# Kernel optimization log

Hardware: AMD Instinct MI355X
Metric: run time of the kernel (lower is better)

Reference implementation:

```python
import jax, jax.numpy as jnp
import numpy as np

MARGIN = 1.0

def setup_inputs() -> dict:
    key = jax.random.key(0)
    k1, k2, k3 = jax.random.split(key, 3)
    B, C, D = 65536, 1000, 512
    x = jax.random.normal(k1, (B, D), dtype=jnp.float32)
    x = x / jnp.linalg.norm(x, axis=1, keepdims=True)  # docstring: ||x||2 = 1
    labels = jax.random.randint(k2, (B,), 0, C, dtype=jnp.int64)
    centers = jax.random.normal(k3, (C, D), dtype=jnp.float32)
    return {"x": x, "labels": labels, "centers": centers}

def reference(x, labels, centers):
    # l2Norm applied to the centers (module is only used when l2Norm is truthy)
    c = centers / jnp.linalg.norm(centers, axis=1, keepdims=True)  # (C, D)
    # cosine distance to every center: one batched GEMM instead of per-sample loop
    dist = 1.0 - jnp.einsum("bd,cd->bc", x, c)                      # (B, C)
    pos = jnp.take_along_axis(dist, labels[:, None], axis=1)[:, 0]  # (B,)
    # min over all classes != label: mask own class with +inf
    same = jnp.arange(c.shape[0])[None, :] == labels[:, None]       # (B, C)
    neg = jnp.min(jnp.where(same, jnp.inf, dist), axis=1)           # (B,)
    # sum of per-sample hinge losses divided by batch size == mean
    return jnp.mean(jax.nn.relu(pos + MARGIN - neg))
```

## Files before the change

kernel.cpp:

```cpp
#include <hip/hip_runtime.h>
#include <stdint.h>

typedef short v8s __attribute__((ext_vector_type(8)));
typedef short v4s __attribute__((ext_vector_type(4)));
typedef float v4f __attribute__((ext_vector_type(4)));

#define BM 128
#define BN 128
#define BK 64
#define POS_INF __builtin_inff()

typedef __attribute__((address_space(3))) unsigned int lds_uint;
typedef const __attribute__((address_space(1))) unsigned int glb_uint;

__device__ __forceinline__ void load16_lds(const void* g, void* l) {
    __builtin_amdgcn_global_load_lds((glb_uint*)g, (lds_uint*)l, 16, 0, 0);
}

__device__ __forceinline__ short f2bf(float f) {
    uint32_t u = __builtin_bit_cast(uint32_t, f);
    u += 0x7fffu + ((u >> 16) & 1u);
    return (short)(u >> 16);
}

__global__ void prep_centers(const float* __restrict__ centers,
                             unsigned short* __restrict__ cbf,
                             int C, int D, float* __restrict__ out) {
    const int row  = blockIdx.x;
    const int lane = threadIdx.x;
    if (row == 0 && lane == 0) out[0] = 0.0f;
    if (row >= C) {
        v4s z = {0, 0, 0, 0};
        for (int d = lane * 4; d < D; d += 256)
            *(v4s*)&cbf[(size_t)row * D + d] = z;
        return;
    }
    const float* src = centers + (size_t)row * D;
    float ss = 0.0f;
    for (int d = lane * 4; d < D; d += 256) {
        v4f f = *(const v4f*)&src[d];
        ss += f.x * f.x + f.y * f.y + f.z * f.z + f.w * f.w;
    }
    #pragma unroll
    for (int off = 32; off; off >>= 1) ss += __shfl_xor(ss, off, 64);
    const float rn = rsqrtf(ss);
    for (int d = lane * 4; d < D; d += 256) {
        v4f f = *(const v4f*)&src[d];
        v4s s;
        s.x = f2bf(f.x * rn); s.y = f2bf(f.y * rn);
        s.z = f2bf(f.z * rn); s.w = f2bf(f.w * rn);
        *(v4s*)&cbf[(size_t)row * D + d] = s;
    }
}

__global__ void convert_x(const float* __restrict__ x,
                          unsigned short* __restrict__ xbf, size_t n) {
    size_t i = ((size_t)blockIdx.x * blockDim.x + threadIdx.x) * 8;
    if (i >= n) return;
    v4f f0 = *(const v4f*)&x[i];
    v4f f1 = *(const v4f*)&x[i + 4];
    v8s s;
    s[0] = f2bf(f0.x); s[1] = f2bf(f0.y); s[2] = f2bf(f0.z); s[3] = f2bf(f0.w);
    s[4] = f2bf(f1.x); s[5] = f2bf(f1.y); s[6] = f2bf(f1.z); s[7] = f2bf(f1.w);
    *(v8s*)&xbf[i] = s;
}

__global__ void gemm_fused(const float* __restrict__ xf,
                           const unsigned short* __restrict__ xbf, int useBf,
                           const unsigned short* __restrict__ cbf,
                           const int* __restrict__ labels,
                           float* __restrict__ pos, float* __restrict__ partial,
                           int Bt, int C, int D, int NT) {
    __shared__ short As[BM * BK];
    __shared__ short Bs[BN * BK];
    __shared__ int   Ls[BM];
    __shared__ float sMinW[2][BM];

    const int t    = threadIdx.x;
    const int nt   = blockIdx.x;
    const int row0 = blockIdx.y * BM;
    const int n0   = nt * BN;

    if (t < BM) Ls[t] = labels[row0 + t];

    const int lane = t & 63;
    const int wave = t >> 6;
    const int wm = wave >> 1, wn = wave & 1;
    const int l15 = lane & 15, q = lane >> 4;

    const int rsub = lane >> 3;
    const int csrc = (lane & 7) ^ rsub;

    v4f acc[4][4];
    #pragma unroll
    for (int i = 0; i < 4; ++i)
        #pragma unroll
        for (int j = 0; j < 4; ++j)
            acc[i][j] = (v4f){0.f, 0.f, 0.f, 0.f};

    const int KT = D / BK;
    for (int kk = 0; kk < KT; ++kk) {
        const int k0 = kk * BK;
        #pragma unroll
        for (int p = 0; p < 4; ++p) {
            const int rbase = wave * 32 + p * 8;
            const unsigned short* g =
                &cbf[(size_t)(n0 + rbase + rsub) * D + k0 + csrc * 8];
            load16_lds(g, &Bs[rbase * BK]);
        }
        if (useBf) {
            #pragma unroll
            for (int p = 0; p < 4; ++p) {
                const int rbase = wave * 32 + p * 8;
                const unsigned short* g =
                    &xbf[(size_t)(row0 + rbase + rsub) * D + k0 + csrc * 8];
                load16_lds(g, &As[rbase * BK]);
            }
        } else {
            #pragma unroll
            for (int p = 0; p < 4; ++p) {
                const int r = (t >> 3) + p * 32;
                const int cs = t & 7;
                const float* src = &xf[(size_t)(row0 + r) * D + k0 + cs * 8];
                v4f f0 = *(const v4f*)&src[0];
                v4f f1 = *(const v4f*)&src[4];
                v8s s;
                s[0] = f2bf(f0.x); s[1] = f2bf(f0.y);
                s[2] = f2bf(f0.z); s[3] = f2bf(f0.w);
                s[4] = f2bf(f1.x); s[5] = f2bf(f1.y);
                s[6] = f2bf(f1.z); s[7] = f2bf(f1.w);
                *(v8s*)&As[r * BK + (cs ^ (r & 7)) * 8] = s;
            }
        }
        __syncthreads();
        #pragma unroll
        for (int ki = 0; ki < BK; ki += 32) {
            const int cbase = ki >> 3;
            v8s a[4], b[4];
            #pragma unroll
            for (int i = 0; i < 4; ++i) {
                const int m = wm * 64 + i * 16 + l15;
                a[i] = *(const v8s*)&As[m * BK + (((cbase + q) ^ (l15 & 7)) * 8)];
            }
            #pragma unroll
            for (int j = 0; j < 4; ++j) {
                const int n = wn * 64 + j * 16 + l15;
                b[j] = *(const v8s*)&Bs[n * BK + (((cbase + q) ^ (l15 & 7)) * 8)];
            }
            #pragma unroll
            for (int i = 0; i < 4; ++i)
                #pragma unroll
                for (int j = 0; j < 4; ++j)
                    acc[i][j] = __builtin_amdgcn_mfma_f32_16x16x32_bf16(
                        a[i], b[j], acc[i][j], 0, 0, 0);
        }
        __syncthreads();
    }

    #pragma unroll
    for (int i = 0; i < 4; ++i) {
        #pragma unroll
        for (int rg = 0; rg < 4; ++rg) {
            const int row_l = wm * 64 + i * 16 + q * 4 + rg;
            const int lab = Ls[row_l];
            float m = POS_INF;
            #pragma unroll
            for (int j = 0; j < 4; ++j) {
                const int col = n0 + wn * 64 + j * 16 + l15;
                const float d = 1.0f - acc[i][j][rg];
                if (col == lab) pos[row0 + row_l] = d;
                else if (col < C) m = fminf(m, d);
            }
            m = fminf(m, __shfl_xor(m, 1, 64));
            m = fminf(m, __shfl_xor(m, 2, 64));
            m = fminf(m, __shfl_xor(m, 4, 64));
            m = fminf(m, __shfl_xor(m, 8, 64));
            if (l15 == 0) sMinW[wn][row_l] = m;
        }
    }
    __syncthreads();
    if (t < BM) {
        const float m = fminf(sMinW[0][t], sMinW[1][t]);
        partial[(size_t)nt * Bt + row0 + t] = m;
    }
}

__global__ void reduce_loss(const float* __restrict__ pos,
                            const float* __restrict__ partial,
                            int Bt, int NT, float margin,
                            float* __restrict__ out) {
    const int r = blockIdx.x * 256 + threadIdx.x;
    float h = 0.0f;
    if (r < Bt) {
        float neg = POS_INF;
        for (int tt = 0; tt < NT; ++tt)
            neg = fminf(neg, partial[(size_t)tt * Bt + r]);
        h = fmaxf(0.0f, pos[r] + margin - neg);
    }
    #pragma unroll
    for (int off = 32; off; off >>= 1) h += __shfl_down(h, off, 64);
    __shared__ float wsum[4];
    const int lane = threadIdx.x & 63, wave = threadIdx.x >> 6;
    if (lane == 0) wsum[wave] = h;
    __syncthreads();
    if (threadIdx.x == 0)
        atomicAdd(out, (wsum[0] + wsum[1] + wsum[2] + wsum[3]) * (1.0f / (float)Bt));
}

extern "C" void kernel_launch(void* const* d_in, const int* in_sizes, int n_in,
                              void* d_out, int out_size, void* d_ws, size_t ws_size,
                              hipStream_t stream) {
    const float* x       = (const float*)d_in[0];
    const int*   labels  = (const int*)d_in[1];
    const float* centers = (const float*)d_in[2];
    float* out = (float*)d_out;

    const int Bt = in_sizes[1];
    const int D  = in_sizes[0] / Bt;
    const int C  = in_sizes[2] / D;
    const int NT = (C + BN - 1) / BN;
    const int CP = NT * BN;

    char* ws = (char*)d_ws;
    unsigned short* cbf = (unsigned short*)ws;
    size_t off = (size_t)CP * D * 2;
    off = (off + 255) & ~(size_t)255;
    float* pos = (float*)(ws + off);      off += (size_t)Bt * 4;
    float* partial = (float*)(ws + off);  off += (size_t)NT * Bt * 4;
    unsigned short* xbf = (unsigned short*)(ws + off);
    const size_t needBig = off + (size_t)Bt * D * 2;
    const int useBf = (ws_size >= needBig) ? 1 : 0;

    prep_centers<<<CP, 64, 0, stream>>>(centers, cbf, C, D, out);
    if (useBf) {
        const size_t n = (size_t)Bt * D;
        convert_x<<<(unsigned)((n / 8 + 255) / 256), 256, 0, stream>>>(x, xbf, n);
    }
    dim3 grid(NT, Bt / BM);
    gemm_fused<<<grid, 256, 0, stream>>>(x, xbf, useBf, cbf, labels, pos, partial,
                                         Bt, C, D, NT);
    reduce_loss<<<(Bt + 255) / 256, 256, 0, stream>>>(pos, partial, Bt, NT, 1.0f, out);
}
```

Before: 298.5 us.

## Remap GEMM blocks per XCD, merge prep kernels, and alias epilogue LDS

The 2D GEMM grid becomes a 1D grid whose block index is decoded so that all eight column tiles of one row block run on the same XCD. Each x tile should then be reused from that XCD's L2 instead of being fetched by eight different XCDs. The centers-normalisation and x-to-bf16 conversion kernels are merged into one launch, with center rows now handled one per wave. The label and min-reduction scratch arrays reuse the GEMM's LDS tiles after the main loop, which shrinks static LDS. The new mapping hardcodes eight column tiles and needs the row-block count to be a multiple of eight, so it holds only for shapes like C=1000.

After: 290.3 us. 2.8% less time.

```diff
diff --git a/kernel.cpp b/kernel.cpp
--- a/kernel.cpp
+++ b/kernel.cpp
@@ -23,46 +23,51 @@
     return (short)(u >> 16);
 }
 
-__global__ void prep_centers(const float* __restrict__ centers,
-                             unsigned short* __restrict__ cbf,
-                             int C, int D, float* __restrict__ out) {
-    const int row  = blockIdx.x;
-    const int lane = threadIdx.x;
-    if (row == 0 && lane == 0) out[0] = 0.0f;
-    if (row >= C) {
-        v4s z = {0, 0, 0, 0};
-        for (int d = lane * 4; d < D; d += 256)
-            *(v4s*)&cbf[(size_t)row * D + d] = z;
-        return;
-    }
-    const float* src = centers + (size_t)row * D;
-    float ss = 0.0f;
-    for (int d = lane * 4; d < D; d += 256) {
-        v4f f = *(const v4f*)&src[d];
-        ss += f.x * f.x + f.y * f.y + f.z * f.z + f.w * f.w;
-    }
-    #pragma unroll
-    for (int off = 32; off; off >>= 1) ss += __shfl_xor(ss, off, 64);
-    const float rn = rsqrtf(ss);
-    for (int d = lane * 4; d < D; d += 256) {
-        v4f f = *(const v4f*)&src[d];
-        v4s s;
-        s.x = f2bf(f.x * rn); s.y = f2bf(f.y * rn);
-        s.z = f2bf(f.z * rn); s.w = f2bf(f.w * rn);
-        *(v4s*)&cbf[(size_t)row * D + d] = s;
-    }
-}
-
-__global__ void convert_x(const float* __restrict__ x,
-                          unsigned short* __restrict__ xbf, size_t n) {
-    size_t i = ((size_t)blockIdx.x * blockDim.x + threadIdx.x) * 8;
-    if (i >= n) return;
-    v4f f0 = *(const v4f*)&x[i];
-    v4f f1 = *(const v4f*)&x[i + 4];
-    v8s s;
-    s[0] = f2bf(f0.x); s[1] = f2bf(f0.y); s[2] = f2bf(f0.z); s[3] = f2bf(f0.w);
-    s[4] = f2bf(f1.x); s[5] = f2bf(f1.y); s[6] = f2bf(f1.z); s[7] = f2bf(f1.w);
-    *(v8s*)&xbf[i] = s;
+__global__ void prep(const float* __restrict__ centers,
+                     unsigned short* __restrict__ cbf,
+                     int C, int D, int CP, int CB,
+                     const float* __restrict__ x,
+                     unsigned short* __restrict__ xbf, size_t nx,
+                     float* __restrict__ out) {
+    const int b = blockIdx.x;
+    const int t = threadIdx.x;
+    if (b == 0 && t == 0) out[0] = 0.0f;
+    if (b < CB) {
+        const int wave = t >> 6, lane = t & 63;
+        const int row = b * 4 + wave;
+        if (row >= CP) return;
+        if (row >= C) {
+            v4s z = {0, 0, 0, 0};
+            for (int d = lane * 4; d < D; d += 256)
+                *(v4s*)&cbf[(size_t)row * D + d] = z;
+            return;
+        }
+        const float* src = centers + (size_t)row * D;
+        float ss = 0.0f;
+        for (int d = lane * 4; d < D; d += 256) {
+            v4f f = *(const v4f*)&src[d];
+            ss += f.x * f.x + f.y * f.y + f.z * f.z + f.w * f.w;
+        }
+        #pragma unroll
+        for (int off = 32; off; off >>= 1) ss += __shfl_xor(ss, off, 64);
+        const float rn = rsqrtf(ss);
+        for (int d = lane * 4; d < D; d += 256) {
+            v4f f = *(const v4f*)&src[d];
+            v4s s;
+            s.x = f2bf(f.x * rn); s.y = f2bf(f.y * rn);
+            s.z = f2bf(f.z * rn); s.w = f2bf(f.w * rn);
+            *(v4s*)&cbf[(size_t)row * D + d] = s;
+        }
+    } else {
+        const size_t i = ((size_t)(b - CB) * 256 + t) * 8;
+        if (i >= nx) return;
+        v4f f0 = *(const v4f*)&x[i];
+        v4f f1 = *(const v4f*)&x[i + 4];
+        v8s s;
+        s[0] = f2bf(f0.x); s[1] = f2bf(f0.y); s[2] = f2bf(f0.z); s[3] = f2bf(f0.w);
+        s[4] = f2bf(f1.x); s[5] = f2bf(f1.y); s[6] = f2bf(f1.z); s[7] = f2bf(f1.w);
+        *(v8s*)&xbf[i] = s;
+    }
 }
 
 __global__ void gemm_fused(const float* __restrict__ xf,
@@ -73,15 +78,15 @@
                            int Bt, int C, int D, int NT) {
     __shared__ short As[BM * BK];
     __shared__ short Bs[BN * BK];
-    __shared__ int   Ls[BM];
-    __shared__ float sMinW[2][BM];
-
-    const int t    = threadIdx.x;
-    const int nt   = blockIdx.x;
-    const int row0 = blockIdx.y * BM;
+
+    const int t   = threadIdx.x;
+    const int bid = blockIdx.x;
+    const int xcd = bid & 7;
+    const int per = bid >> 3;
+    const int rowblk = (per >> 3) * 8 + xcd;
+    const int nt     = per & 7;
+    const int row0 = rowblk * BM;
     const int n0   = nt * BN;
-
-    if (t < BM) Ls[t] = labels[row0 + t];
 
     const int lane = t & 63;
     const int wave = t >> 6;
@@ -157,6 +162,11 @@
         __syncthreads();
     }
 
+    int*   Ls    = (int*)As;
+    float* sMinW = (float*)Bs;
+    if (t < BM) Ls[t] = labels[row0 + t];
+    __syncthreads();
+
     #pragma unroll
     for (int i = 0; i < 4; ++i) {
         #pragma unroll
@@ -175,12 +185,12 @@
             m = fminf(m, __shfl_xor(m, 2, 64));
             m = fminf(m, __shfl_xor(m, 4, 64));
             m = fminf(m, __shfl_xor(m, 8, 64));
-            if (l15 == 0) sMinW[wn][row_l] = m;
+            if (l15 == 0) sMinW[wn * BM + row_l] = m;
         }
     }
     __syncthreads();
     if (t < BM) {
-        const float m = fminf(sMinW[0][t], sMinW[1][t]);
+        const float m = fminf(sMinW[t], sMinW[BM + t]);
         partial[(size_t)nt * Bt + row0 + t] = m;
     }
 }
@@ -220,6 +230,7 @@
     const int C  = in_sizes[2] / D;
     const int NT = (C + BN - 1) / BN;
     const int CP = NT * BN;
+    const int NB = Bt / BM;
 
     char* ws = (char*)d_ws;
     unsigned short* cbf = (unsigned short*)ws;
@@ -231,13 +242,12 @@
     const size_t needBig = off + (size_t)Bt * D * 2;
     const int useBf = (ws_size >= needBig) ? 1 : 0;
 
-    prep_centers<<<CP, 64, 0, stream>>>(centers, cbf, C, D, out);
-    if (useBf) {
-        const size_t n = (size_t)Bt * D;
-        convert_x<<<(unsigned)((n / 8 + 255) / 256), 256, 0, stream>>>(x, xbf, n);
-    }
-    dim3 grid(NT, Bt / BM);
-    gemm_fused<<<grid, 256, 0, stream>>>(x, xbf, useBf, cbf, labels, pos, partial,
-                                         Bt, C, D, NT);
+    const size_t nx = (size_t)Bt * D;
+    const int CB = CP / 4;
+    const int XB = useBf ? (int)((nx / 8 + 255) / 256) : 0;
+    prep<<<CB + XB, 256, 0, stream>>>(centers, cbf, C, D, CP, CB, x, xbf, nx, out);
+
+    gemm_fused<<<NB * NT, 256, 0, stream>>>(x, xbf, useBf, cbf, labels, pos,
+                                            partial, Bt, C, D, NT);
     reduce_loss<<<(Bt + 255) / 256, 256, 0, stream>>>(pos, partial, Bt, NT, 1.0f, out);
 }
```
